# Performance work log

Measured on AMD Instinct MI355X. Metric: run time of the kernel, lower is better.

The kernel has to match this reference:

```python
import jax, jax.numpy as jnp
import numpy as np

DISTANCE_THRESHOLD = 100.0  # squared-distance threshold (cdist**2 <= thresh)
NO_CODE_ID = -1


def setup_inputs() -> dict:
    key = jax.random.key(0)
    kx, kc = jax.random.split(key)
    x = jax.random.normal(kx, (2, 1024, 64), dtype=jnp.float32)      # [b, s, d] query tokens
    codes = jax.random.normal(kc, (50000, 64), dtype=jnp.float32)    # [n, d] active code bank
    return {"x": x, "codes": codes}


def reference(x, codes):
    # squared euclidean distances, matching torch.cdist(x, codes) ** 2
    x2 = jnp.sum(x * x, axis=-1, keepdims=True)            # [b, s, 1]
    c2 = jnp.sum(codes * codes, axis=-1)                   # [n]
    cross = jnp.einsum('bsd,nd->bsn', x, codes)            # [b, s, n]
    d2 = jnp.maximum(x2 + c2 - 2.0 * cross, 0.0)           # clamp tiny negatives, cdist >= 0

    within = jnp.any(d2 <= DISTANCE_THRESHOLD, axis=-1)    # [b, s]
    nn_ids = jnp.argmin(d2, axis=-1)                       # [b, s]
    return jnp.where(within, nn_ids, NO_CODE_ID)
```

## Files before the change

kernel.cpp:

```cpp
#include <hip/hip_runtime.h>

#define NTOK   2048
#define DIM    64
#define NCODES 50000
#define THRESH 100.0f
#define BIG    3.0e38f
#define MARGIN 4.0f
#define NBLK   391
#define BM32   1564
#define BM32P  1568

typedef __attribute__((ext_vector_type(8)))  __bf16 bf16x8;
typedef __attribute__((ext_vector_type(16))) float  float16;

__device__ __forceinline__ unsigned short f2bf(float f) {
    union { float f; unsigned int u; } v; v.f = f;
    unsigned int r = v.u + 0x7FFF + ((v.u >> 16) & 1);
    return (unsigned short)(r >> 16);
}
__device__ __forceinline__ unsigned int pack2(float a, float b) {
    return (unsigned int)f2bf(a) | ((unsigned int)f2bf(b) << 16);
}

__global__ __launch_bounds__(256)
void nn_prep_kernel(const float* __restrict__ x, const float* __restrict__ codes,
                    unsigned short* __restrict__ cbf, unsigned short* __restrict__ xbf,
                    float* __restrict__ c2, float* __restrict__ x2,
                    float* __restrict__ bm32) {
    int g = blockIdx.x * 256 + threadIdx.x;
    if (g < NTOK * 4) {
        int t = g >> 2;
        bm32[(size_t)t * BM32P + BM32 + (g & 3)] = BIG;
    }
    int row = g >> 2;
    int seg = g & 3;
    const float* src;
    unsigned short* dst;
    float* nrm;
    if (row < NCODES) {
        src = codes + (size_t)row * DIM + seg * 16;
        dst = cbf + (size_t)row * DIM + seg * 16;
        nrm = (seg == 0) ? (c2 + row) : nullptr;
    } else if (row < NCODES + NTOK) {
        int r = row - NCODES;
        src = x + (size_t)r * DIM + seg * 16;
        dst = xbf + (size_t)r * DIM + seg * 16;
        nrm = (seg == 0) ? (x2 + r) : nullptr;
    } else {
        return;
    }
    float4 v0 = ((const float4*)src)[0];
    float4 v1 = ((const float4*)src)[1];
    float4 v2 = ((const float4*)src)[2];
    float4 v3 = ((const float4*)src)[3];
    float s = 0.f;
    s = fmaf(v0.x, v0.x, s); s = fmaf(v0.y, v0.y, s);
    s = fmaf(v0.z, v0.z, s); s = fmaf(v0.w, v0.w, s);
    s = fmaf(v1.x, v1.x, s); s = fmaf(v1.y, v1.y, s);
    s = fmaf(v1.z, v1.z, s); s = fmaf(v1.w, v1.w, s);
    s = fmaf(v2.x, v2.x, s); s = fmaf(v2.y, v2.y, s);
    s = fmaf(v2.z, v2.z, s); s = fmaf(v2.w, v2.w, s);
    s = fmaf(v3.x, v3.x, s); s = fmaf(v3.y, v3.y, s);
    s = fmaf(v3.z, v3.z, s); s = fmaf(v3.w, v3.w, s);
    uint4 lo, hi;
    lo.x = pack2(v0.x, v0.y); lo.y = pack2(v0.z, v0.w);
    lo.z = pack2(v1.x, v1.y); lo.w = pack2(v1.z, v1.w);
    hi.x = pack2(v2.x, v2.y); hi.y = pack2(v2.z, v2.w);
    hi.z = pack2(v3.x, v3.y); hi.w = pack2(v3.z, v3.w);
    *(uint4*)dst = lo;
    *(uint4*)(dst + 8) = hi;
    s += __shfl_xor(s, 1);
    s += __shfl_xor(s, 2);
    if (nrm) *nrm = s;
}

__global__ __launch_bounds__(256, 2)
void nn_stageA_kernel(const unsigned short* __restrict__ xbf,
                      const unsigned short* __restrict__ cbf,
                      const float* __restrict__ c2g,
                      float* __restrict__ bm32) {
    __shared__ __bf16 xs[256 * 72];
    __shared__ __bf16 cs[128 * 72];
    __shared__ float  c2s[128];

    const int tid  = threadIdx.x;
    const int w    = tid >> 6;
    const int lane = tid & 63;
    const int l31  = lane & 31;
    const int h    = lane >> 5;
    const int t0   = blockIdx.x * 256;
    const int n0   = blockIdx.y * 128;

#pragma unroll
    for (int it = 0; it < 4; ++it) {
        int g = it * 256 + tid;
        int row = g >> 3, seg = g & 7;
        int n = n0 + row;
        uint4 v = make_uint4(0, 0, 0, 0);
        if (n < NCODES) v = *(const uint4*)(cbf + (size_t)n * DIM + seg * 8);
        *(uint4*)&cs[row * 72 + seg * 8] = v;
    }
#pragma unroll
    for (int it = 0; it < 8; ++it) {
        int g = it * 256 + tid;
        int row = g >> 3, seg = g & 7;
        uint4 v = *(const uint4*)(xbf + (size_t)(t0 + row) * DIM + seg * 8);
        *(uint4*)&xs[row * 72 + seg * 8] = v;
    }
    if (tid < 128) {
        int n = n0 + tid;
        c2s[tid] = (n < NCODES) ? c2g[n] : BIG;
    }
    __syncthreads();

    float16 acc[4][2];
#pragma unroll
    for (int mi = 0; mi < 4; ++mi) {
#pragma unroll
        for (int g2 = 0; g2 < 4; ++g2) {
            float4 c4 = *(float4*)&c2s[mi * 32 + g2 * 8 + 4 * h];
#pragma unroll
            for (int i = 0; i < 4; ++i) {
                float iv = -0.5f * ((float*)&c4)[i];
                acc[mi][0][g2 * 4 + i] = iv;
                acc[mi][1][g2 * 4 + i] = iv;
            }
        }
    }

#pragma unroll
    for (int s = 0; s < 4; ++s) {
        bf16x8 a[4], b[2];
#pragma unroll
        for (int mi = 0; mi < 4; ++mi)
            a[mi] = *(bf16x8*)&cs[(mi * 32 + l31) * 72 + s * 16 + h * 8];
#pragma unroll
        for (int nj = 0; nj < 2; ++nj)
            b[nj] = *(bf16x8*)&xs[(w * 64 + nj * 32 + l31) * 72 + s * 16 + h * 8];
#pragma unroll
        for (int mi = 0; mi < 4; ++mi)
#pragma unroll
            for (int nj = 0; nj < 2; ++nj)
                acc[mi][nj] = __builtin_amdgcn_mfma_f32_32x32x16_bf16(
                    a[mi], b[nj], acc[mi][nj], 0, 0, 0);
    }

#pragma unroll
    for (int nj = 0; nj < 2; ++nj) {
#pragma unroll
        for (int mi = 0; mi < 4; ++mi) {
            float m = acc[mi][nj][0];
#pragma unroll
            for (int r = 1; r < 16; ++r) m = fmaxf(m, acc[mi][nj][r]);
            m = fmaxf(m, __shfl_xor(m, 32));
            if (lane < 32) {
                int token = t0 + w * 64 + nj * 32 + lane;
                bm32[(size_t)token * BM32P + blockIdx.y * 4 + mi] = -2.0f * m;
            }
        }
    }
}

__global__ __launch_bounds__(256)
void nn_finalize_kernel(const float* __restrict__ x,
                        const float* __restrict__ codes,
                        const float* __restrict__ c2,
                        const float* __restrict__ x2,
                        const float* __restrict__ bm32,
                        int* __restrict__ out) {
    __shared__ float redf[8];
    __shared__ int   redi[4];
    __shared__ int   queue[BM32P];
    __shared__ int   qcount;
    __shared__ float gshare;

    const int tid  = threadIdx.x;
    const int w    = tid >> 6;
    const int lane = tid & 63;
    const int t    = blockIdx.x;
    const float* bm = bm32 + (size_t)t * BM32P;

    if (tid == 0) qcount = 0;

    float v[7];
    float g = BIG;
#pragma unroll
    for (int k = 0; k < 7; ++k) {
        int b = tid + k * 256;
        v[k] = (b < BM32P) ? bm[b] : BIG;
        g = fminf(g, v[k]);
    }
#pragma unroll
    for (int m = 1; m < 64; m <<= 1) g = fminf(g, __shfl_xor(g, m));
    if (lane == 0) redf[w] = g;
    __syncthreads();
    if (tid == 0)
        gshare = fminf(fminf(redf[0], redf[1]), fminf(redf[2], redf[3])) + MARGIN;
    __syncthreads();
    const float th = gshare;

#pragma unroll
    for (int k = 0; k < 7; ++k) {
        int b = tid + k * 256;
        if (b < BM32P && v[k] <= th) {
            int slot = atomicAdd(&qcount, 1);
            queue[slot] = b;
        }
    }
    __syncthreads();
    const int nq = qcount;

    const int half = lane & 1;
    float4 xh[8];
#pragma unroll
    for (int q = 0; q < 8; ++q)
        xh[q] = *(const float4*)(x + (size_t)t * DIM + half * 32 + q * 4);
    const float x2v = x2[t];

    float bv = BIG;
    int   bi = 0x7fffffff;
    for (int e = w; e < nq; e += 4) {
        int blk = queue[e];
        int n = blk * 32 + (lane >> 1);
        if (n < NCODES) {
            const float4* cp = (const float4*)(codes + (size_t)n * DIM + half * 32);
            float d = 0.f;
#pragma unroll
            for (int q = 0; q < 8; ++q) {
                float4 c4 = cp[q];
                d = fmaf(xh[q].x, c4.x, d);
                d = fmaf(xh[q].y, c4.y, d);
                d = fmaf(xh[q].z, c4.z, d);
                d = fmaf(xh[q].w, c4.w, d);
            }
            d += __shfl_xor(d, 1);
            float d2 = fmaxf(fmaf(-2.f, d, x2v + c2[n]), 0.f);
            if (d2 < bv || (d2 == bv && n < bi)) { bv = d2; bi = n; }
        }
    }
#pragma unroll
    for (int m = 1; m < 64; m <<= 1) {
        float vv = __shfl_xor(bv, m);
        int   ii = __shfl_xor(bi, m);
        if (vv < bv || (vv == bv && ii < bi)) { bv = vv; bi = ii; }
    }
    if (lane == 0) { redf[4 + w] = bv; redi[w] = bi; }
    __syncthreads();
    if (tid == 0) {
        float fb = BIG;
        int   fi = 0x7fffffff;
#pragma unroll
        for (int i = 0; i < 4; ++i) {
            float vv = redf[4 + i];
            int   ii = redi[i];
            if (vv < fb || (vv == fb && ii < fi)) { fb = vv; fi = ii; }
        }
        out[t] = (fb <= THRESH) ? fi : -1;
    }
}

extern "C" void kernel_launch(void* const* d_in, const int* in_sizes, int n_in,
                              void* d_out, int out_size, void* d_ws, size_t ws_size,
                              hipStream_t stream) {
    const float* x     = (const float*)d_in[0];
    const float* codes = (const float*)d_in[1];

    float* c2 = (float*)d_ws;
    float* x2 = c2 + 50048;
    unsigned short* cbf = (unsigned short*)(x2 + NTOK);
    unsigned short* xbf = cbf + (size_t)NCODES * DIM;
    float* bm32 = (float*)(xbf + (size_t)NTOK * DIM);
    int* out = (int*)d_out;

    nn_prep_kernel<<<814, 256, 0, stream>>>(x, codes, cbf, xbf, c2, x2, bm32);
    nn_stageA_kernel<<<dim3(8, NBLK), 256, 0, stream>>>(xbf, cbf, c2, bm32);
    nn_finalize_kernel<<<NTOK, 256, 0, stream>>>(x, codes, c2, x2, bm32, out);
}
```

Before: 122.9 us.

## Make stage-A blocks persistent over code tiles with register prefetch and resident token fragments

Stage A now launches 56x8 blocks, each looping over up to 7 code tiles instead of one block per code tile. The token bf16 fragments are loaded once into registers rather than staged through shared memory. The next code tile is prefetched into registers while the current tile computes. This cuts redundant token loads and per-block launch overhead and overlaps global loads with MFMA work, at the cost of fewer blocks (448) for the GPU and more register pressure.

```diff
diff --git a/kernel.cpp b/kernel.cpp
--- a/kernel.cpp
+++ b/kernel.cpp
@@ -9,6 +9,7 @@
 #define NBLK   391
 #define BM32   1564
 #define BM32P  1568
+#define NCG    56
 
 typedef __attribute__((ext_vector_type(8)))  __bf16 bf16x8;
 typedef __attribute__((ext_vector_type(16))) float  float16;
@@ -79,7 +80,6 @@
                       const unsigned short* __restrict__ cbf,
                       const float* __restrict__ c2g,
                       float* __restrict__ bm32) {
-    __shared__ __bf16 xs[256 * 72];
     __shared__ __bf16 cs[128 * 72];
     __shared__ float  c2s[128];
 
@@ -88,74 +88,92 @@
     const int lane = tid & 63;
     const int l31  = lane & 31;
     const int h    = lane >> 5;
-    const int t0   = blockIdx.x * 256;
-    const int n0   = blockIdx.y * 128;
-
-#pragma unroll
-    for (int it = 0; it < 4; ++it) {
-        int g = it * 256 + tid;
-        int row = g >> 3, seg = g & 7;
-        int n = n0 + row;
-        uint4 v = make_uint4(0, 0, 0, 0);
-        if (n < NCODES) v = *(const uint4*)(cbf + (size_t)n * DIM + seg * 8);
-        *(uint4*)&cs[row * 72 + seg * 8] = v;
-    }
-#pragma unroll
-    for (int it = 0; it < 8; ++it) {
-        int g = it * 256 + tid;
-        int row = g >> 3, seg = g & 7;
-        uint4 v = *(const uint4*)(xbf + (size_t)(t0 + row) * DIM + seg * 8);
-        *(uint4*)&xs[row * 72 + seg * 8] = v;
-    }
-    if (tid < 128) {
-        int n = n0 + tid;
-        c2s[tid] = (n < NCODES) ? c2g[n] : BIG;
-    }
-    __syncthreads();
-
-    float16 acc[4][2];
-#pragma unroll
-    for (int mi = 0; mi < 4; ++mi) {
-#pragma unroll
-        for (int g2 = 0; g2 < 4; ++g2) {
-            float4 c4 = *(float4*)&c2s[mi * 32 + g2 * 8 + 4 * h];
-#pragma unroll
-            for (int i = 0; i < 4; ++i) {
-                float iv = -0.5f * ((float*)&c4)[i];
-                acc[mi][0][g2 * 4 + i] = iv;
-                acc[mi][1][g2 * 4 + i] = iv;
+    const int g0   = blockIdx.x * 7;
+    const int nb   = min(7, NBLK - g0);
+    const int t0   = blockIdx.y * 256;
+
+    bf16x8 bfr[4][2];
+#pragma unroll
+    for (int s = 0; s < 4; ++s)
+#pragma unroll
+        for (int nj = 0; nj < 2; ++nj)
+            bfr[s][nj] = *(const bf16x8*)&xbf[
+                (size_t)(t0 + w * 64 + nj * 32 + l31) * DIM + s * 16 + h * 8];
+
+    uint4 pr[4];
+    float prc;
+    auto prefetch = [&](int blk) {
+        int n0 = blk * 128;
+#pragma unroll
+        for (int it = 0; it < 4; ++it) {
+            int g = it * 256 + tid;
+            int row = g >> 3, seg = g & 7;
+            int n = n0 + row;
+            pr[it] = (n < NCODES) ? *(const uint4*)(cbf + (size_t)n * DIM + seg * 8)
+                                  : make_uint4(0, 0, 0, 0);
+        }
+        if (tid < 128) {
+            int n = n0 + tid;
+            prc = (n < NCODES) ? c2g[n] : BIG;
+        }
+    };
+    prefetch(g0);
+
+    for (int t = 0; t < nb; ++t) {
+        const int blk = g0 + t;
+        __syncthreads();
+
+#pragma unroll
+        for (int it = 0; it < 4; ++it) {
+            int g = it * 256 + tid;
+            int row = g >> 3, seg = g & 7;
+            *(uint4*)&cs[row * 72 + seg * 8] = pr[it];
+        }
+        if (tid < 128) c2s[tid] = prc;
+        if (t + 1 < nb) prefetch(blk + 1);
+        __syncthreads();
+
+        float16 acc[4][2];
+#pragma unroll
+        for (int mi = 0; mi < 4; ++mi) {
+#pragma unroll
+            for (int g2 = 0; g2 < 4; ++g2) {
+                float4 c4 = *(float4*)&c2s[mi * 32 + g2 * 8 + 4 * h];
+#pragma unroll
+                for (int i = 0; i < 4; ++i) {
+                    float iv = -0.5f * ((float*)&c4)[i];
+                    acc[mi][0][g2 * 4 + i] = iv;
+                    acc[mi][1][g2 * 4 + i] = iv;
+                }
             }
         }
-    }
-
-#pragma unroll
-    for (int s = 0; s < 4; ++s) {
-        bf16x8 a[4], b[2];
-#pragma unroll
-        for (int mi = 0; mi < 4; ++mi)
-            a[mi] = *(bf16x8*)&cs[(mi * 32 + l31) * 72 + s * 16 + h * 8];
-#pragma unroll
-        for (int nj = 0; nj < 2; ++nj)
-            b[nj] = *(bf16x8*)&xs[(w * 64 + nj * 32 + l31) * 72 + s * 16 + h * 8];
-#pragma unroll
-        for (int mi = 0; mi < 4; ++mi)
-#pragma unroll
-            for (int nj = 0; nj < 2; ++nj)
-                acc[mi][nj] = __builtin_amdgcn_mfma_f32_32x32x16_bf16(
-                    a[mi], b[nj], acc[mi][nj], 0, 0, 0);
-    }
-
-#pragma unroll
-    for (int nj = 0; nj < 2; ++nj) {
-#pragma unroll
-        for (int mi = 0; mi < 4; ++mi) {
-            float m = acc[mi][nj][0];
-#pragma unroll
-            for (int r = 1; r < 16; ++r) m = fmaxf(m, acc[mi][nj][r]);
-            m = fmaxf(m, __shfl_xor(m, 32));
-            if (lane < 32) {
-                int token = t0 + w * 64 + nj * 32 + lane;
-                bm32[(size_t)token * BM32P + blockIdx.y * 4 + mi] = -2.0f * m;
+
+#pragma unroll
+        for (int s = 0; s < 4; ++s) {
+            bf16x8 a[4];
+#pragma unroll
+            for (int mi = 0; mi < 4; ++mi)
+                a[mi] = *(bf16x8*)&cs[(mi * 32 + l31) * 72 + s * 16 + h * 8];
+#pragma unroll
+            for (int mi = 0; mi < 4; ++mi)
+#pragma unroll
+                for (int nj = 0; nj < 2; ++nj)
+                    acc[mi][nj] = __builtin_amdgcn_mfma_f32_32x32x16_bf16(
+                        a[mi], bfr[s][nj], acc[mi][nj], 0, 0, 0);
+        }
+
+#pragma unroll
+        for (int nj = 0; nj < 2; ++nj) {
+#pragma unroll
+            for (int mi = 0; mi < 4; ++mi) {
+                float m = acc[mi][nj][0];
+#pragma unroll
+                for (int r = 1; r < 16; ++r) m = fmaxf(m, acc[mi][nj][r]);
+                m = fmaxf(m, __shfl_xor(m, 32));
+                if (lane < 32) {
+                    int token = t0 + w * 64 + nj * 32 + lane;
+                    bm32[(size_t)token * BM32P + blk * 4 + mi] = -2.0f * m;
+                }
             }
         }
     }
@@ -273,6 +291,6 @@
     int* out = (int*)d_out;
 
     nn_prep_kernel<<<814, 256, 0, stream>>>(x, codes, cbf, xbf, c2, x2, bm32);
-    nn_stageA_kernel<<<dim3(8, NBLK), 256, 0, stream>>>(xbf, cbf, c2, bm32);
+    nn_stageA_kernel<<<dim3(NCG, 8), 256, 0, stream>>>(xbf, cbf, c2, bm32);
     nn_finalize_kernel<<<NTOK, 256, 0, stream>>>(x, codes, c2, x2, bm32, out);
 }
```

After: 113.2 us. 7.9% less time.
